# Kernel tuning notes

Hardware: AMD Instinct MI355X
Metric: run time of the kernel (lower is better)

## Reference

```python
import jax, jax.numpy as jnp
import numpy as np

IMG_H = 256; IMG_W = 256; N_PTS = 192
MIN_DEPTH = 3.0; MAX_DEPTH = 9.0
NDC_EXTENT = 1.0; FOCAL = 4.0  # focal length so rays at volume center span ~[-1,1]
EPS = 1e-8; EA_EPS = 1e-10


def setup_inputs() -> dict:
    key = jax.random.key(0)
    image3d = jax.random.uniform(key, (1, 1, 128, 128, 128), dtype=jnp.float32)
    R = jnp.eye(3, dtype=jnp.float32)[None]            # [1,3,3] camera rotation
    T = jnp.array([[0.0, 0.0, 4.0]], dtype=jnp.float32)  # camera center at world (0,0,-4)
    return {"image3d": image3d, "R": R, "T": T}


def _trilinear(vol, pts):
    # vol: [C,D,H,W]; pts: [N,3] xyz in [-1,1]; align_corners=True, zero padding
    C, D, H, W = vol.shape
    fx = (pts[:, 0] + 1.0) * 0.5 * (W - 1)
    fy = (pts[:, 1] + 1.0) * 0.5 * (H - 1)
    fz = (pts[:, 2] + 1.0) * 0.5 * (D - 1)
    x0 = jnp.floor(fx); y0 = jnp.floor(fy); z0 = jnp.floor(fz)
    wx = fx - x0; wy = fy - y0; wz = fz - z0
    out = jnp.zeros((pts.shape[0], C), vol.dtype)
    for dz in (0, 1):
        for dy in (0, 1):
            for dx in (0, 1):
                xi = x0 + dx; yi = y0 + dy; zi = z0 + dz
                w = ((wx if dx else 1.0 - wx) * (wy if dy else 1.0 - wy)
                     * (wz if dz else 1.0 - wz))
                valid = ((xi >= 0) & (xi <= W - 1) & (yi >= 0) & (yi <= H - 1)
                         & (zi >= 0) & (zi <= D - 1))
                xc = jnp.clip(xi, 0, W - 1).astype(jnp.int32)
                yc = jnp.clip(yi, 0, H - 1).astype(jnp.int32)
                zc = jnp.clip(zi, 0, D - 1).astype(jnp.int32)
                vals = vol[:, zc, yc, xc]          # [C,N] gather
                out = out + (w * valid).astype(vol.dtype)[:, None] * vals.T
    return out                                      # [N,C]


def reference(image3d, R, T):
    B = image3d.shape[0]
    features = jnp.repeat(image3d, 3, axis=1)                 # [B,3,D,H,W]
    densities = jnp.ones_like(image3d) / N_PTS                # [B,1,D,H,W]
    vol4 = jnp.concatenate([features, densities], axis=1)     # [B,4,D,H,W]
    # NDC pixel grid + depths along each ray
    ys = jnp.linspace(1.0, -1.0, IMG_H)
    xs = jnp.linspace(1.0, -1.0, IMG_W)
    yg, xg = jnp.meshgrid(ys, xs, indexing="ij")              # [H,W]
    depths = jnp.linspace(MIN_DEPTH, MAX_DEPTH, N_PTS)        # [P]
    x_cam = xg[..., None] * depths / FOCAL                    # [H,W,P]
    y_cam = yg[..., None] * depths / FOCAL
    z_cam = jnp.broadcast_to(depths, x_cam.shape)
    pts_cam = jnp.stack([x_cam, y_cam, z_cam], axis=-1)       # [H,W,P,3]
    # X_cam = X_world @ R + T  =>  X_world = (X_cam - T) @ R^T
    pts_world = jnp.einsum("bhwpj,bij->bhwpi",
                           pts_cam[None] - T[:, None, None, None, :], R)
    local = pts_world / NDC_EXTENT                            # volume local coords in [-1,1]
    sampled = jax.vmap(_trilinear)(vol4, local.reshape(B, -1, 3))  # [B,N,4]
    sampled = sampled.reshape(B, IMG_H, IMG_W, N_PTS, 4)
    feats = sampled[..., :3]
    dens = sampled[..., 3]                                    # [B,H,W,P]
    # EmissionAbsorption raymarcher (shifted cumprod of transmittance)
    t = (1.0 + EA_EPS) - dens
    cp = jnp.cumprod(t, axis=-1)
    absorption = jnp.concatenate([jnp.ones_like(cp[..., :1]), cp[..., :-1]], axis=-1)
    weights = dens * absorption
    rgb = jnp.einsum("bhwp,bhwpc->bhwc", weights, feats)      # [B,H,W,3]
    opac = 1.0 - jnp.prod(1.0 - dens, axis=-1, keepdims=True)
    rgba = jnp.concatenate([rgb, opac], axis=-1)              # [B,H,W,4]
    screen = jnp.transpose(rgba, (0, 3, 1, 2))                # [B,4,H,W]
    gray = screen.mean(axis=1, keepdims=True)                 # [B,1,H,W]
    # normalized(standardized(x))  (torch std is unbiased -> ddof=1)
    std = (gray - gray.mean()) / (jnp.std(gray, ddof=1) + EPS)
    out = (std - std.min() + EPS) / (std.max() - std.min() + EPS)
    return out
```

## Files before the change

kernel.cpp:

```cpp
#include <hip/hip_runtime.h>
#include <math.h>

#define N_PIX (256 * 256)
#define N_PTS 192
#define SEGS 8
#define TILE_PIX 64
#define N_BLK (N_PIX / TILE_PIX)
#define THREADS (TILE_PIX * SEGS)

#define L2Q  (-0.0075336725f)
#define QF   (0.99479166677f)

__device__ __forceinline__ void general_step(
    const float* __restrict__ vol, float pf,
    float A0, float B0, float A1, float B1, float A2, float B2,
    float& S, float& Prun)
{
    const float fx = fmaf(A0, pf, B0);
    const float fy = fmaf(A1, pf, B1);
    const float fz = fmaf(A2, pf, B2);
    const float x0f = floorf(fx), y0f = floorf(fy), z0f = floorf(fz);
    const float wx = fx - x0f, wy = fy - y0f, wz = fz - z0f;
    const int ix = (int)x0f, iy = (int)y0f, iz = (int)z0f;
    const float ax0 = (ix >= 0  && ix <= 127) ? (1.0f - wx) : 0.0f;
    const float ax1 = (ix >= -1 && ix <= 126) ? wx : 0.0f;
    const float ay0 = (iy >= 0  && iy <= 127) ? (1.0f - wy) : 0.0f;
    const float ay1 = (iy >= -1 && iy <= 126) ? wy : 0.0f;
    const float az0 = (iz >= 0  && iz <= 127) ? (1.0f - wz) : 0.0f;
    const float az1 = (iz >= -1 && iz <= 126) ? wz : 0.0f;
    const float s = (ax0 + ax1) * (ay0 + ay1) * (az0 + az1);
    const float dens = s * (1.0f / 192.0f);
    const int xc0 = min(max(ix, 0), 127), xc1 = min(max(ix + 1, 0), 127);
    const int yc0 = min(max(iy, 0), 127), yc1 = min(max(iy + 1, 0), 127);
    const int zc0 = min(max(iz, 0), 127), zc1 = min(max(iz + 1, 0), 127);
    const float* q00 = vol + (zc0 * 128 + yc0) * 128;
    const float* q01 = vol + (zc0 * 128 + yc1) * 128;
    const float* q10 = vol + (zc1 * 128 + yc0) * 128;
    const float* q11 = vol + (zc1 * 128 + yc1) * 128;
    const float feat =
        az0 * (ay0 * (ax0 * q00[xc0] + ax1 * q00[xc1]) +
               ay1 * (ax0 * q01[xc0] + ax1 * q01[xc1])) +
        az1 * (ay0 * (ax0 * q10[xc0] + ax1 * q10[xc1]) +
               ay1 * (ax0 * q11[xc0] + ax1 * q11[xc1]));
    S = fmaf(dens * Prun, feat, S);
    Prun *= (1.0f + 1e-10f - dens);
}

__global__ __launch_bounds__(THREADS) void render_kernel(
    const float* __restrict__ vol,
    const float* __restrict__ Rm,
    const float* __restrict__ Tv,
    float* __restrict__ out,
    float* __restrict__ part)
{
    const int tid = threadIdx.x;
    const int seg = tid >> 6;
    const int l   = tid & 63;
    const int tr  = blockIdx.x >> 5;
    const int tc  = blockIdx.x & 31;
    const int h = tr * 8 + (l >> 3);
    const int w = tc * 8 + (l & 7);
    const float yg = 1.0f - (2.0f / 255.0f) * (float)h;
    const float xg = 1.0f - (2.0f / 255.0f) * (float)w;

    const float r00 = Rm[0], r01 = Rm[1], r02 = Rm[2];
    const float r10 = Rm[3], r11 = Rm[4], r12 = Rm[5];
    const float r20 = Rm[6], r21 = Rm[7], r22 = Rm[8];
    const float t0 = Tv[0], t1 = Tv[1], t2 = Tv[2];

    const float a0 = 0.25f * (r00 * xg + r01 * yg) + r02;
    const float a1 = 0.25f * (r10 * xg + r11 * yg) + r12;
    const float a2 = 0.25f * (r20 * xg + r21 * yg) + r22;
    const float b0 = -(r00 * t0 + r01 * t1 + r02 * t2);
    const float b1 = -(r10 * t0 + r11 * t1 + r12 * t2);
    const float b2 = -(r20 * t0 + r21 * t1 + r22 * t2);

    const float step = 6.0f / 191.0f;
    const float rstep = 191.0f / 6.0f;

    const float A0 = a0 * step * 63.5f, B0 = (fmaf(a0, 3.0f, b0) + 1.0f) * 63.5f;
    const float A1 = a1 * step * 63.5f, B1 = (fmaf(a1, 3.0f, b1) + 1.0f) * 63.5f;
    const float A2 = a2 * step * 63.5f, B2 = (fmaf(a2, 3.0f, b2) + 1.0f) * 63.5f;

    const float LIM = 1.0f + 2.0f / 127.0f + 1e-4f;
    const float WHI = 1.0f - 1e-5f;
    float dlo = 3.0f, dhi = 9.0f;
    float dloI = 3.0f, dhiI = 9.0f;
    {
        const float aa[3] = {a0, a1, a2};
        const float bb[3] = {b0, b1, b2};
        #pragma unroll
        for (int k = 0; k < 3; ++k) {
            const float a = aa[k], b = bb[k];
            if (fabsf(a) > 1e-12f) {
                const float ra = 1.0f / a;
                const float o0 = (-LIM - b) * ra, o1 = (LIM - b) * ra;
                dlo = fmaxf(dlo, fminf(o0, o1));
                dhi = fminf(dhi, fmaxf(o0, o1));
                const float i0 = (-1.0f - b) * ra, i1 = (WHI - b) * ra;
                dloI = fmaxf(dloI, fminf(i0, i1));
                dhiI = fminf(dhiI, fmaxf(i0, i1));
            } else {
                if (fabsf(b) >= LIM) dhi = -1e30f;
                if (b < -1.0f || b > WHI) dhiI = -1e30f;
            }
        }
    }
    int plo = (int)ceilf((dlo - 3.0f) * rstep - 1e-3f);
    int phi = (int)floorf((dhi - 3.0f) * rstep + 1e-3f);
    plo = max(plo, 0);
    phi = min(phi, N_PTS - 1);
    int len = phi - plo + 1;
    if (len < 0) { len = 0; phi = plo - 1; }
    int plo2 = (int)ceilf((dloI - 3.0f) * rstep + 1e-3f);
    int phi2 = (int)floorf((dhiI - 3.0f) * rstep - 1e-3f);
    plo2 = max(plo2, plo);
    phi2 = min(phi2, phi);
    if (plo2 > phi2) { plo2 = phi + 1; phi2 = phi; }

    const int chunk = (len + SEGS - 1) >> 3;
    const int beg = plo + seg * chunk;
    const int end = min(beg + chunk, plo + len);

    float Prun = 1.0f;
    float S = 0.0f;

    const int aEnd = min(end, plo2);
    for (int p = beg; p < aEnd; ++p)
        general_step(vol, (float)p, A0, B0, A1, B1, A2, B2, S, Prun);

    const int i0b = max(beg, plo2);
    const int i1b = min(end, phi2 + 1);
    float qp = 1.0f, S2 = 0.0f;
    #pragma unroll 4
    for (int p = i0b; p < i1b; ++p) {
        const float pf = (float)p;
        const float fx = fmaf(A0, pf, B0);
        const float fy = fmaf(A1, pf, B1);
        const float fz = fmaf(A2, pf, B2);
        const float x0f = floorf(fx), y0f = floorf(fy), z0f = floorf(fz);
        const float wx = fx - x0f, wy = fy - y0f, wz = fz - z0f;
        const int ix = (int)x0f, iy = (int)y0f, iz = (int)z0f;
        const float* q0 = vol + ((iz * 128 + iy) * 128 + ix);
        const float v000 = q0[0],     v001 = q0[1];
        const float v010 = q0[128],   v011 = q0[129];
        const float v100 = q0[16384], v101 = q0[16385];
        const float v110 = q0[16512], v111 = q0[16513];
        const float x00 = fmaf(wx, v001 - v000, v000);
        const float x01 = fmaf(wx, v011 - v010, v010);
        const float x10 = fmaf(wx, v101 - v100, v100);
        const float x11 = fmaf(wx, v111 - v110, v110);
        const float y0v = fmaf(wy, x01 - x00, x00);
        const float y1v = fmaf(wy, x11 - x10, x10);
        const float feat = fmaf(wz, y1v - y0v, y0v);
        S2 = fmaf(qp, feat, S2);
        qp *= QF;
    }
    if (i1b > i0b) {
        const int kint = i1b - i0b;
        S = fmaf(Prun * (1.0f / 192.0f), S2, S);
        Prun *= exp2f((float)kint * L2Q);
    }

    const int bBeg = max(beg, phi2 + 1);
    for (int p = bBeg; p < end; ++p)
        general_step(vol, (float)p, A0, B0, A1, B1, A2, B2, S, Prun);

    __shared__ float sP[SEGS][TILE_PIX];
    __shared__ float sS[SEGS][TILE_PIX];
    sP[seg][l] = Prun;
    sS[seg][l] = S;
    __syncthreads();

    if (tid < TILE_PIX) {
        float absorb = 1.0f, wS = 0.0f;
        #pragma unroll
        for (int s = 0; s < SEGS; ++s) {
            wS = fmaf(absorb, sS[s][l], wS);
            absorb *= sP[s][l];
        }
        const float g = (3.0f * wS + (1.0f - absorb)) * 0.25f;
        out[h * 256 + w] = g;

        float vs = g, vq = g * g, vmn = g, vmx = g;
        #pragma unroll
        for (int off = 1; off < 64; off <<= 1) {
            vs += __shfl_xor(vs, off);
            vq += __shfl_xor(vq, off);
            vmn = fminf(vmn, __shfl_xor(vmn, off));
            vmx = fmaxf(vmx, __shfl_xor(vmx, off));
        }
        if (l == 0) {
            part[blockIdx.x]             = vs;
            part[N_BLK + blockIdx.x]     = vq;
            part[2 * N_BLK + blockIdx.x] = vmn;
            part[3 * N_BLK + blockIdx.x] = vmx;
        }
    }
}

__global__ __launch_bounds__(256) void finish_kernel(
    float* __restrict__ out,
    const float* __restrict__ part)
{
    const int tid = threadIdx.x;
    __shared__ float s_s[4], s_q[4], s_n[4], s_x[4];
    __shared__ float s_fin[4];

    float fs  = part[tid]               + part[tid + 256]
              + part[tid + 512]         + part[tid + 768];
    float fq  = part[N_BLK + tid]       + part[N_BLK + tid + 256]
              + part[N_BLK + tid + 512] + part[N_BLK + tid + 768];
    float fn  = fminf(fminf(part[2 * N_BLK + tid],       part[2 * N_BLK + tid + 256]),
                      fminf(part[2 * N_BLK + tid + 512], part[2 * N_BLK + tid + 768]));
    float fx2 = fmaxf(fmaxf(part[3 * N_BLK + tid],       part[3 * N_BLK + tid + 256]),
                      fmaxf(part[3 * N_BLK + tid + 512], part[3 * N_BLK + tid + 768]));
    #pragma unroll
    for (int off = 1; off < 64; off <<= 1) {
        fs += __shfl_xor(fs, off);
        fq += __shfl_xor(fq, off);
        fn  = fminf(fn,  __shfl_xor(fn, off));
        fx2 = fmaxf(fx2, __shfl_xor(fx2, off));
    }
    const int wave = tid >> 6;
    const int lane = tid & 63;
    if (lane == 0) { s_s[wave] = fs; s_q[wave] = fq; s_n[wave] = fn; s_x[wave] = fx2; }
    __syncthreads();
    if (tid == 0) {
        const float tsum = s_s[0] + s_s[1] + s_s[2] + s_s[3];
        const float tsq  = s_q[0] + s_q[1] + s_q[2] + s_q[3];
        const float tmn  = fminf(fminf(s_n[0], s_n[1]), fminf(s_n[2], s_n[3]));
        const float tmx  = fmaxf(fmaxf(s_x[0], s_x[1]), fmaxf(s_x[2], s_x[3]));
        const float N = (float)N_PIX;
        const float mean = tsum / N;
        float var = (tsq - N * mean * mean) / (N - 1.0f);
        if (var < 0.0f) var = 0.0f;
        const float denom = sqrtf(var) + 1e-8f;
        s_fin[0] = mean;
        s_fin[1] = denom;
        s_fin[2] = (tmn - mean) / denom;
        s_fin[3] = (tmx - mean) / denom;
    }
    __syncthreads();

    const float mean = s_fin[0];
    const float rdenom = 1.0f / s_fin[1];
    const float smin = s_fin[2];
    const float rrange = 1.0f / (s_fin[3] - smin + 1e-8f);
    const int i = blockIdx.x * 256 + tid;
    const float sv = (out[i] - mean) * rdenom;
    out[i] = (sv - smin + 1e-8f) * rrange;
}

extern "C" void kernel_launch(void* const* d_in, const int* in_sizes, int n_in,
                              void* d_out, int out_size, void* d_ws, size_t ws_size,
                              hipStream_t stream)
{
    const float* vol = (const float*)d_in[0];
    const float* Rm  = (const float*)d_in[1];
    const float* Tv  = (const float*)d_in[2];
    float* out = (float*)d_out;
    float* part = (float*)d_ws;

    hipLaunchKernelGGL(render_kernel, dim3(N_BLK), dim3(THREADS), 0, stream,
                       vol, Rm, Tv, out, part);
    hipLaunchKernelGGL(finish_kernel, dim3(N_PIX / 256), dim3(256), 0, stream,
                       out, part);
}
```

Before: 78.34 us.

## Pre-pack volume into fp16 2x2 neighbor quads for trilinear gathers

A new pre-pass kernel converts the float volume into a layout where each voxel stores its 2x2 (x,y) neighborhood as four halves in one 8-byte word. The render loops then fetch two 8-byte loads per sample instead of eight scattered 4-byte loads. This cuts the number of gather instructions per sample. In exchange it adds a 16 MB write pass every call, doubles the footprint in cache, and lowers feature precision to fp16.

```diff
diff --git a/kernel.cpp b/kernel.cpp
--- a/kernel.cpp
+++ b/kernel.cpp
@@ -1,4 +1,5 @@
 #include <hip/hip_runtime.h>
+#include <hip/hip_fp16.h>
 #include <math.h>
 
 #define N_PIX (256 * 256)
@@ -7,12 +8,32 @@
 #define TILE_PIX 64
 #define N_BLK (N_PIX / TILE_PIX)
 #define THREADS (TILE_PIX * SEGS)
+#define VOL_ELEMS (128 * 128 * 128)
 
 #define L2Q  (-0.0075336725f)
 #define QF   (0.99479166677f)
 
+__global__ __launch_bounds__(256) void pack_kernel(
+    const float* __restrict__ vol, uint2* __restrict__ volq)
+{
+    const int idx = blockIdx.x * 256 + threadIdx.x;
+    const int x = idx & 127;
+    const int y = (idx >> 7) & 127;
+    const int z = idx >> 14;
+    const int x1 = min(x + 1, 127);
+    const int y1 = min(y + 1, 127);
+    const float* r0 = vol + (z * 128 + y ) * 128;
+    const float* r1 = vol + (z * 128 + y1) * 128;
+    const __half2 lo = __floats2half2_rn(r0[x], r0[x1]);
+    const __half2 hi = __floats2half2_rn(r1[x], r1[x1]);
+    uint2 o;
+    o.x = *(const unsigned int*)&lo;
+    o.y = *(const unsigned int*)&hi;
+    volq[idx] = o;
+}
+
 __device__ __forceinline__ void general_step(
-    const float* __restrict__ vol, float pf,
+    const uint2* __restrict__ volq, float pf,
     float A0, float B0, float A1, float B1, float A2, float B2,
     float& S, float& Prun)
 {
@@ -30,24 +51,29 @@
     const float az1 = (iz >= -1 && iz <= 126) ? wz : 0.0f;
     const float s = (ax0 + ax1) * (ay0 + ay1) * (az0 + az1);
     const float dens = s * (1.0f / 192.0f);
-    const int xc0 = min(max(ix, 0), 127), xc1 = min(max(ix + 1, 0), 127);
-    const int yc0 = min(max(iy, 0), 127), yc1 = min(max(iy + 1, 0), 127);
-    const int zc0 = min(max(iz, 0), 127), zc1 = min(max(iz + 1, 0), 127);
-    const float* q00 = vol + (zc0 * 128 + yc0) * 128;
-    const float* q01 = vol + (zc0 * 128 + yc1) * 128;
-    const float* q10 = vol + (zc1 * 128 + yc0) * 128;
-    const float* q11 = vol + (zc1 * 128 + yc1) * 128;
-    const float feat =
-        az0 * (ay0 * (ax0 * q00[xc0] + ax1 * q00[xc1]) +
-               ay1 * (ax0 * q01[xc0] + ax1 * q01[xc1])) +
-        az1 * (ay0 * (ax0 * q10[xc0] + ax1 * q10[xc1]) +
-               ay1 * (ax0 * q11[xc0] + ax1 * q11[xc1]));
+    int xi = ix; float wx0 = ax0, wx1 = ax1;
+    if (xi < 0) { xi = 0; wx0 = ax1; wx1 = 0.0f; } else { xi = min(xi, 127); }
+    int yi = iy; float wy0 = ay0, wy1 = ay1;
+    if (yi < 0) { yi = 0; wy0 = ay1; wy1 = 0.0f; } else { yi = min(yi, 127); }
+    const int zc0 = min(max(iz, 0), 127);
+    const int zc1 = min(max(iz + 1, 0), 127);
+    const uint2 A = volq[(zc0 * 128 + yi) * 128 + xi];
+    const uint2 B = volq[(zc1 * 128 + yi) * 128 + xi];
+    const float2 a0 = __half22float2(*(const __half2*)&A.x);
+    const float2 a1 = __half22float2(*(const __half2*)&A.y);
+    const float2 b0 = __half22float2(*(const __half2*)&B.x);
+    const float2 b1 = __half22float2(*(const __half2*)&B.y);
+    const float bl0 = wy0 * (wx0 * a0.x + wx1 * a0.y)
+                    + wy1 * (wx0 * a1.x + wx1 * a1.y);
+    const float bl1 = wy0 * (wx0 * b0.x + wx1 * b0.y)
+                    + wy1 * (wx0 * b1.x + wx1 * b1.y);
+    const float feat = az0 * bl0 + az1 * bl1;
     S = fmaf(dens * Prun, feat, S);
     Prun *= (1.0f + 1e-10f - dens);
 }
 
 __global__ __launch_bounds__(THREADS) void render_kernel(
-    const float* __restrict__ vol,
+    const uint2* __restrict__ volq,
     const float* __restrict__ Rm,
     const float* __restrict__ Tv,
     float* __restrict__ out,
@@ -127,7 +153,7 @@
 
     const int aEnd = min(end, plo2);
     for (int p = beg; p < aEnd; ++p)
-        general_step(vol, (float)p, A0, B0, A1, B1, A2, B2, S, Prun);
+        general_step(volq, (float)p, A0, B0, A1, B1, A2, B2, S, Prun);
 
     const int i0b = max(beg, plo2);
     const int i1b = min(end, phi2 + 1);
@@ -141,15 +167,17 @@
         const float x0f = floorf(fx), y0f = floorf(fy), z0f = floorf(fz);
         const float wx = fx - x0f, wy = fy - y0f, wz = fz - z0f;
         const int ix = (int)x0f, iy = (int)y0f, iz = (int)z0f;
-        const float* q0 = vol + ((iz * 128 + iy) * 128 + ix);
-        const float v000 = q0[0],     v001 = q0[1];
-        const float v010 = q0[128],   v011 = q0[129];
-        const float v100 = q0[16384], v101 = q0[16385];
-        const float v110 = q0[16512], v111 = q0[16513];
-        const float x00 = fmaf(wx, v001 - v000, v000);
-        const float x01 = fmaf(wx, v011 - v010, v010);
-        const float x10 = fmaf(wx, v101 - v100, v100);
-        const float x11 = fmaf(wx, v111 - v110, v110);
+        const int base = (iz * 128 + iy) * 128 + ix;
+        const uint2 A = volq[base];
+        const uint2 B = volq[base + 16384];
+        const float2 a0v = __half22float2(*(const __half2*)&A.x);
+        const float2 a1v = __half22float2(*(const __half2*)&A.y);
+        const float2 b0v = __half22float2(*(const __half2*)&B.x);
+        const float2 b1v = __half22float2(*(const __half2*)&B.y);
+        const float x00 = fmaf(wx, a0v.y - a0v.x, a0v.x);
+        const float x01 = fmaf(wx, a1v.y - a1v.x, a1v.x);
+        const float x10 = fmaf(wx, b0v.y - b0v.x, b0v.x);
+        const float x11 = fmaf(wx, b1v.y - b1v.x, b1v.x);
         const float y0v = fmaf(wy, x01 - x00, x00);
         const float y1v = fmaf(wy, x11 - x10, x10);
         const float feat = fmaf(wz, y1v - y0v, y0v);
@@ -164,7 +192,7 @@
 
     const int bBeg = max(beg, phi2 + 1);
     for (int p = bBeg; p < end; ++p)
-        general_step(vol, (float)p, A0, B0, A1, B1, A2, B2, S, Prun);
+        general_step(volq, (float)p, A0, B0, A1, B1, A2, B2, S, Prun);
 
     __shared__ float sP[SEGS][TILE_PIX];
     __shared__ float sS[SEGS][TILE_PIX];
@@ -260,10 +288,13 @@
     const float* Rm  = (const float*)d_in[1];
     const float* Tv  = (const float*)d_in[2];
     float* out = (float*)d_out;
-    float* part = (float*)d_ws;
-
+    uint2* volq = (uint2*)d_ws;
+    float* part = (float*)((char*)d_ws + VOL_ELEMS * 8);
+
+    hipLaunchKernelGGL(pack_kernel, dim3(VOL_ELEMS / 256), dim3(256), 0, stream,
+                       vol, volq);
     hipLaunchKernelGGL(render_kernel, dim3(N_BLK), dim3(THREADS), 0, stream,
-                       vol, Rm, Tv, out, part);
+                       volq, Rm, Tv, out, part);
     hipLaunchKernelGGL(finish_kernel, dim3(N_PIX / 256), dim3(256), 0, stream,
                        out, part);
 }
```

New measurement: 83.30 us. +6.3%, slower.
